# Kernel optimization log

Hardware: AMD Instinct MI355X
Metric: run time of the kernel (lower is better)

Reference implementation:

```python
import jax, jax.numpy as jnp
import numpy as np
import math

N_EMBD = 1024
N_HEAD = 16
BLOCK = 2048
SPARSITY = 0.25
B, T = 2, 2048


def _make_mask_logits(rng):
    # Replicates the patterned init in SparseMixtureAttention.__init__.
    S = BLOCK
    logits = np.empty((N_HEAD, S, S), dtype=np.float32)
    for h in range(N_HEAD):
        if h % 3 == 0:  # banded pattern (bandwidth 16)
            i = np.arange(S)
            band = (np.abs(i[:, None] - i[None, :]) <= 16)
            logits[h] = np.where(band, rng.standard_normal((S, S)) + 2.0,
                                 rng.standard_normal((S, S)) - 2.0)
        elif h % 3 == 1:  # strided pattern: every 4th column
            strided = (np.arange(S)[None, :] % 4 == 0)
            logits[h] = np.where(strided, rng.standard_normal((S, S)) + 2.0,
                                 rng.standard_normal((S, S)) - 2.0)
        else:  # random pattern with given sparsity
            rnd = rng.random((S, S)) < SPARSITY
            logits[h] = np.where(rnd, rng.standard_normal((S, S)) + 2.0,
                                 rng.standard_normal((S, S)) - 2.0)
    # keep the diagonal unmasked so no causal row is fully masked (avoids NaN rows)
    d = np.arange(S)
    logits[:, d, d] = np.abs(logits[:, d, d]) + 2.0
    return logits.astype(np.float32)


def setup_inputs() -> dict:
    key = jax.random.key(0)
    ks = jax.random.split(key, 5)
    rng = np.random.default_rng(0)
    return {
        "x": jax.random.normal(ks[0], (B, T, N_EMBD), dtype=jnp.float32),
        "mask_logits": jnp.asarray(_make_mask_logits(rng)),
        "W_attn": jax.random.normal(ks[1], (3 * N_EMBD, N_EMBD), dtype=jnp.float32) * 0.02,
        "b_attn": jnp.zeros((3 * N_EMBD,), dtype=jnp.float32),
        "W_proj": jax.random.normal(ks[2], (N_EMBD, N_EMBD), dtype=jnp.float32) * 0.02,
        "b_proj": jnp.zeros((N_EMBD,), dtype=jnp.float32),
    }


def reference(x, mask_logits, W_attn, b_attn, W_proj, b_proj):
    Bx, Tx, C = x.shape
    H = mask_logits.shape[0]
    D = C // H
    qkv = x @ W_attn.T + b_attn                       # [B,T,3C]
    q, k, v = jnp.split(qkv, 3, axis=-1)
    q = q.reshape(Bx, Tx, H, D)
    k = k.reshape(Bx, Tx, H, D)
    v = v.reshape(Bx, Tx, H, D)
    att = jnp.einsum('bthd,bshd->bhts', q, k) * (1.0 / math.sqrt(D))  # [B,H,T,T]
    # forward value of the STE mask equals the hard mask (probs - probs.detach() == 0)
    keep = jax.nn.sigmoid(mask_logits[:, :Tx, :Tx]) > 0.5             # [H,T,T]
    causal = jnp.tril(jnp.ones((Tx, Tx), dtype=bool))
    mask = causal[None, :, :] & keep                                  # [H,T,T]
    att = jnp.where(mask[None], att, -jnp.inf)
    att = jax.nn.softmax(att, axis=-1)
    y = jnp.einsum('bhts,bshd->bthd', att, v).reshape(Bx, Tx, C)
    return y @ W_proj.T + b_proj
```

## Files before the change

### kernel.cpp

```cpp
#include <hip/hip_runtime.h>
#include <hip/hip_bf16.h>
#include <stdint.h>

typedef unsigned short u16;
typedef unsigned int u32;
typedef unsigned long long u64;
typedef __attribute__((ext_vector_type(8))) short bf16x8;
typedef __attribute__((ext_vector_type(4))) float f32x4;

#define NB 2
#define NH 16
#define TT 2048
#define DD 64
#define CC 1024

__device__ __forceinline__ u16 bf16bits(float f) {
    __hip_bfloat16 h = __float2bfloat16(f);
    return __builtin_bit_cast(unsigned short, h);
}

__device__ __forceinline__ void gload_lds16(const void* g, void* l) {
    __builtin_amdgcn_global_load_lds(
        (const __attribute__((address_space(1))) void*)g,
        (__attribute__((address_space(3))) void*)l, 16, 0, 0);
}

__global__ __launch_bounds__(256) void prep_all(
    const float* __restrict__ x, const float* __restrict__ Wa_f,
    const float* __restrict__ Wp_f, const float* __restrict__ ml,
    u16* __restrict__ xb, u16* __restrict__ wab, u16* __restrict__ wpb,
    unsigned char* __restrict__ mb) {
    const int bid = blockIdx.x;
    if (bid < 512) {
        int idx = bid * 256 + threadIdx.x;
        for (int i = idx; i < 2097152; i += 512 * 256) {
            const float* src; u16* dst; int off;
            if (i < 1048576)      { src = x;    dst = xb;  off = i; }
            else if (i < 1835008) { src = Wa_f; dst = wab; off = i - 1048576; }
            else                  { src = Wp_f; dst = wpb; off = i - 1835008; }
            float4 v = reinterpret_cast<const float4*>(src)[off];
            ushort4 o;
            o.x = bf16bits(v.x); o.y = bf16bits(v.y);
            o.z = bf16bits(v.z); o.w = bf16bits(v.w);
            reinterpret_cast<ushort4*>(dst)[off] = o;
        }
    } else {
        const int wid = ((bid - 512) << 2) + (threadIdx.x >> 6);
        const int lane = threadIdx.x & 63;
        const int i0 = wid & 2047;
        const int hbase = (wid >> 11) << 3;
#pragma unroll 1
        for (int k = 0; k < 8; ++k) {
            int h = hbase + k;
            int i = (k & 1) ? (2047 - i0) : i0;
            int row = h * 2048 + i;
            const float* src = ml + (size_t)row * TT;
            unsigned char* dst = mb + (size_t)row * (TT / 8);
#pragma unroll 1
            for (int c8 = lane; c8 < 256; c8 += 64) {
                unsigned char v = 0;
                if (c8 * 8 <= i) {
                    const float4* p = reinterpret_cast<const float4*>(src + c8 * 8);
                    float4 a = p[0];
                    float4 b = p[1];
                    unsigned u = 0;
                    u |= (a.x > 0.f) ? 1u : 0u;
                    u |= (a.y > 0.f) ? 2u : 0u;
                    u |= (a.z > 0.f) ? 4u : 0u;
                    u |= (a.w > 0.f) ? 8u : 0u;
                    u |= (b.x > 0.f) ? 16u : 0u;
                    u |= (b.y > 0.f) ? 32u : 0u;
                    u |= (b.z > 0.f) ? 64u : 0u;
                    u |= (b.w > 0.f) ? 128u : 0u;
                    int rem = i - c8 * 8;
                    if (rem < 7) u &= (1u << (rem + 1)) - 1;
                    v = (unsigned char)u;
                }
                dst[c8] = v;
            }
        }
    }
}

template <int MODE>
__global__ __launch_bounds__(256) void gemm_bt(
    const u16* __restrict__ A, const u16* __restrict__ Bw,
    const float* __restrict__ bias,
    u16* __restrict__ Qb, u16* __restrict__ Kb, u16* __restrict__ Vtb,
    float* __restrict__ Cout, int Kdim) {
    const int bm = blockIdx.y * 128;
    const int bn = blockIdx.x * 128;
    const int tid = threadIdx.x;
    const int w = tid >> 6, lane = tid & 63;
    const int lrow = lane & 15, lgrp = lane >> 4;
    const int wr = (w >> 1) * 64, wc = (w & 1) * 64;

    __shared__ __align__(16) u16 ABs[2][128 * 64];
    u16* As = ABs[0];
    u16* Bs = ABs[1];

    f32x4 acc[4][4] = {};

    const int nkt = Kdim >> 6;
    for (int kt = 0; kt < nkt; ++kt) {
        const int k0 = kt << 6;
#pragma unroll
        for (int i = 0; i < 4; ++i) {
            int e = i * 2048 + tid * 8;
            int r = e >> 6, c = e & 63;
            gload_lds16(A + (size_t)(bm + r) * Kdim + k0 + c, (char*)As + i * 4096 + w * 1024);
            gload_lds16(Bw + (size_t)(bn + r) * Kdim + k0 + c, (char*)Bs + i * 4096 + w * 1024);
        }
        __syncthreads();
#pragma unroll
        for (int kk = 0; kk < 2; ++kk) {
            bf16x8 af[4], bfz[4];
#pragma unroll
            for (int i = 0; i < 4; ++i)
                af[i] = *reinterpret_cast<const bf16x8*>(&As[(wr + i * 16 + lrow) * 64 + kk * 32 + lgrp * 8]);
#pragma unroll
            for (int i = 0; i < 4; ++i)
                bfz[i] = *reinterpret_cast<const bf16x8*>(&Bs[(wc + i * 16 + lrow) * 64 + kk * 32 + lgrp * 8]);
#pragma unroll
            for (int mi = 0; mi < 4; ++mi)
#pragma unroll
                for (int ni = 0; ni < 4; ++ni)
                    acc[mi][ni] = __builtin_amdgcn_mfma_f32_16x16x32_bf16(af[mi], bfz[ni], acc[mi][ni], 0, 0, 0);
        }
        __syncthreads();
    }

    const int sec = (MODE == 0) ? (bn >> 10) : 1;

    if (MODE == 0 && sec == 2) {
        u16* Tl = &ABs[0][0];
#pragma unroll
        for (int ni = 0; ni < 4; ++ni) {
            int nl = wc + ni * 16 + lrow;
            float bv = bias[bn + nl];
#pragma unroll
            for (int mi = 0; mi < 4; ++mi) {
                int ml2 = wr + mi * 16 + lgrp * 4;
                u64 pk = 0;
#pragma unroll
                for (int j = 0; j < 4; ++j)
                    pk |= (u64)bf16bits(acc[mi][ni][j] + bv) << (16 * j);
                int byte = nl * 256 + ((ml2 * 2) ^ ((nl & 7) << 4));
                *reinterpret_cast<u64*>((char*)Tl + byte) = pk;
            }
        }
        __syncthreads();
        int r = tid >> 1, half = tid & 1;
        int h = ((bn & 1023) >> 6) + (r >> 6);
        int d = r & 63;
        int b = bm >> 11;
        u16* gdst = Vtb + (((size_t)b * NH + h) * DD + d) * TT + (bm & 2047) + half * 64;
#pragma unroll
        for (int c = 0; c < 8; ++c) {
            uint4 v = *reinterpret_cast<const uint4*>(
                (char*)Tl + r * 256 + ((half * 128 + c * 16) ^ ((r & 7) << 4)));
            *reinterpret_cast<uint4*>(gdst + c * 8) = v;
        }
        return;
    }

#pragma unroll
    for (int ni = 0; ni < 4; ++ni) {
        int n = bn + wc + ni * 16 + lrow;
        float bv = bias[n];
#pragma unroll
        for (int mi = 0; mi < 4; ++mi) {
#pragma unroll
            for (int j = 0; j < 4; ++j) {
                int m = bm + wr + mi * 16 + lgrp * 4 + j;
                float v = acc[mi][ni][j] + bv;
                if (MODE == 1) {
                    Cout[(size_t)m * 1024 + n] = v;
                } else {
                    int h = (n & 1023) >> 6;
                    int d = n & 63;
                    int b = m >> 11;
                    int t = m & 2047;
                    if (sec == 0) {
                        Qb[(((size_t)b * NH + h) * TT + t) * DD + d] =
                            bf16bits(v * (0.125f * 1.4426950408889634f));
                    } else {
                        Kb[(((size_t)b * NH + h) * TT + t) * DD + d] = bf16bits(v);
                    }
                }
            }
        }
    }
}

__global__ __launch_bounds__(256) void attn_kernel(
    const u16* __restrict__ Qb, const u16* __restrict__ Kb,
    const u16* __restrict__ Vtb, const unsigned char* __restrict__ mb,
    u16* __restrict__ att_out) {
    const int slot = blockIdx.x >> 4;
    const int h = blockIdx.x & 15;
    const int b = blockIdx.y;
    const int qt = (slot < 16) ? (31 - slot) : (slot - 16);
    const int tid = threadIdx.x;
    const int w = tid >> 6, lane = tid & 63;
    const int lrow = lane & 15, g = lane >> 4;

    __shared__ __align__(16) u16 Ks[2][64 * 64];
    __shared__ __align__(16) u16 Vts[2][64 * 64];
    __shared__ __align__(16) u16 Ps[4][16 * 64];

    const u16* kg_base = &Kb[((size_t)b * NH + h) * TT * DD];
    const u16* vg_base = &Vtb[((size_t)b * NH + h) * DD * TT];

    auto STAGE = [&](int bufi, int kt) {
#pragma unroll
        for (int i = 0; i < 2; ++i) {
            int e = i * 2048 + tid * 8;
            int r = e >> 6, c = e & 63;
            int cs = c ^ ((r & 7) << 3);
            gload_lds16(kg_base + (size_t)kt * 64 * DD + r * DD + cs,
                        (char*)Ks[bufi] + i * 4096 + w * 1024);
            gload_lds16(vg_base + kt * 64 + (size_t)r * TT + cs,
                        (char*)Vts[bufi] + i * 4096 + w * 1024);
        }
    };

    const int qrow_g = qt * 64 + w * 16 + lrow;
    const int rswz = (lrow & 7) << 4;

    bf16x8 qf[2];
#pragma unroll
    for (int kk = 0; kk < 2; ++kk)
        qf[kk] = *reinterpret_cast<const bf16x8*>(
            &Qb[(((size_t)b * NH + h) * TT + qrow_g) * DD + kk * 32 + g * 8]);

    f32x4 oacc[4] = {};
    float l_run = 0.f;

    const unsigned char* mrow_base = mb + ((size_t)h * TT + qrow_g) * (TT / 8);
    char* PsW = (char*)&Ps[w][0];

    STAGE(0, 0);
    int buf = 0;

#pragma unroll 1
    for (int kt = 0; kt <= qt; ++kt) {
        u64 mw = *reinterpret_cast<const u64*>(mrow_base + kt * 8);
        if (kt < qt) {
            STAGE(buf ^ 1, kt + 1);
            asm volatile("s_waitcnt vmcnt(5)" ::: "memory");
        } else {
            asm volatile("s_waitcnt vmcnt(1)" ::: "memory");
        }
        __builtin_amdgcn_sched_barrier(0);
        asm volatile("s_barrier" ::: "memory");

        f32x4 s[4] = {};
        __builtin_amdgcn_s_setprio(1);
#pragma unroll
        for (int kk = 0; kk < 2; ++kk)
#pragma unroll
            for (int nt = 0; nt < 4; ++nt) {
                bf16x8 kf = *reinterpret_cast<const bf16x8*>(
                    (char*)Ks[buf] + (((nt * 16 + lrow) * 128 + (kk * 32 + g * 8) * 2) ^ rswz));
                s[nt] = __builtin_amdgcn_mfma_f32_16x16x32_bf16(kf, qf[kk], s[nt], 0, 0, 0);
            }
        __builtin_amdgcn_s_setprio(0);

        u64 mws = mw >> (g * 4);
        u32 wlo = (u32)mws, whi = (u32)(mws >> 32);
        float rs = 0.f;
#pragma unroll
        for (int nt = 0; nt < 4; ++nt)
#pragma unroll
            for (int j = 0; j < 4; ++j) {
                int bi = nt * 16 + j;
                u32 word = (bi < 32) ? wlo : whi;
                u32 pm = (u32)(((int)(word << (31 - (bi & 31)))) >> 31);
                float p = __builtin_bit_cast(float,
                          __builtin_bit_cast(u32, exp2f(s[nt][j])) & pm);
                rs += p;
                s[nt][j] = p;
            }
        rs += __shfl_xor(rs, 16);
        rs += __shfl_xor(rs, 32);
        l_run += rs;

#pragma unroll
        for (int nt = 0; nt < 4; ++nt)
#pragma unroll
            for (int t = 0; t < 2; ++t) {
                u32 pk = (u32)bf16bits(s[nt][2 * t]) |
                         ((u32)bf16bits(s[nt][2 * t + 1]) << 16);
                int byte = (lrow * 128 + (nt * 16 + g * 4 + 2 * t) * 2) ^ rswz;
                *reinterpret_cast<u32*>(PsW + byte) = pk;
            }

        __builtin_amdgcn_s_setprio(1);
#pragma unroll
        for (int kk = 0; kk < 2; ++kk) {
            bf16x8 pf = *reinterpret_cast<const bf16x8*>(
                PsW + ((lrow * 128 + (kk * 32 + g * 8) * 2) ^ rswz));
#pragma unroll
            for (int dt = 0; dt < 4; ++dt) {
                bf16x8 vf = *reinterpret_cast<const bf16x8*>(
                    (char*)Vts[buf] + (((dt * 16 + lrow) * 128 + (kk * 32 + g * 8) * 2) ^ rswz));
                oacc[dt] = __builtin_amdgcn_mfma_f32_16x16x32_bf16(pf, vf, oacc[dt], 0, 0, 0);
            }
        }
        __builtin_amdgcn_s_setprio(0);

        asm volatile("s_barrier" ::: "memory");
        buf ^= 1;
    }

    float lb[4];
#pragma unroll
    for (int j = 0; j < 4; ++j)
        lb[j] = __shfl(l_run, (lane & 48) + g * 4 + j);
#pragma unroll
    for (int dt = 0; dt < 4; ++dt)
#pragma unroll
        for (int j = 0; j < 4; ++j) {
            int t = qt * 64 + w * 16 + g * 4 + j;
            float o = oacc[dt][j] / lb[j];
            att_out[((size_t)b * TT + t) * CC + h * DD + dt * 16 + lrow] = bf16bits(o);
        }
}

extern "C" void kernel_launch(void* const* d_in, const int* in_sizes, int n_in,
                              void* d_out, int out_size, void* d_ws, size_t ws_size,
                              hipStream_t stream) {
    const float* x = (const float*)d_in[0];
    const float* mask_logits = (const float*)d_in[1];
    const float* W_attn = (const float*)d_in[2];
    const float* b_attn = (const float*)d_in[3];
    const float* W_proj = (const float*)d_in[4];
    const float* b_proj = (const float*)d_in[5];
    float* out = (float*)d_out;

    char* ws = (char*)d_ws;
    u16* xb  = (u16*)(ws + 0);
    u16* Wa  = (u16*)(ws + (8u << 20));
    u16* Wp  = (u16*)(ws + (14u << 20));
    u16* Qb  = (u16*)(ws + (16u << 20));
    u16* Kb  = (u16*)(ws + (24u << 20));
    u16* Vtb = (u16*)(ws + (32u << 20));
    u16* att = (u16*)(ws + (40u << 20));
    unsigned char* mbits = (unsigned char*)(ws + (48u << 20));

    prep_all<<<1536, 256, 0, stream>>>(x, W_attn, W_proj, mask_logits,
                                       xb, Wa, Wp, mbits);
    gemm_bt<0><<<dim3(24, 32), 256, 0, stream>>>(xb, Wa, b_attn, Qb, Kb, Vtb, nullptr, CC);
    attn_kernel<<<dim3(512, 2), 256, 0, stream>>>(Qb, Kb, Vtb, mbits, att);
    gemm_bt<1><<<dim3(8, 32), 256, 0, stream>>>(att, Wp, b_proj, nullptr, nullptr, nullptr, out, CC);
}
```

Baseline: 161.4 us.

## Process two query tiles per block and split long causal rows across blocks

Each attention block now handles 128 query rows as two 64-row tiles that share each staged K/V tile, which halves K/V LDS staging per query row. Long causal rows (query chunks 8-15) are split across two blocks over the key range; these write unnormalised bf16 partial outputs and row sums to workspace, and a new combine kernel sums them and normalises. The aim is better load balance across 768 blocks and reuse of K/V loads. The cost is an extra kernel launch, extra bf16 rounding of the partials, and higher register pressure under the 3-waves launch bound. The partials reuse workspace regions that earlier kernels have already finished with.

```diff
diff --git a/kernel.cpp b/kernel.cpp
--- a/kernel.cpp
+++ b/kernel.cpp
@@ -17,6 +17,11 @@
 __device__ __forceinline__ u16 bf16bits(float f) {
     __hip_bfloat16 h = __float2bfloat16(f);
     return __builtin_bit_cast(unsigned short, h);
+}
+
+__device__ __forceinline__ float bf2f(u16 u) {
+    u32 x = (u32)u << 16;
+    return __builtin_bit_cast(float, x);
 }
 
 __device__ __forceinline__ void gload_lds16(const void* g, void* l) {
@@ -193,21 +198,28 @@
     }
 }
 
-__global__ __launch_bounds__(256) void attn_kernel(
+__global__ __launch_bounds__(256, 3) void attn_kernel(
     const u16* __restrict__ Qb, const u16* __restrict__ Kb,
     const u16* __restrict__ Vtb, const unsigned char* __restrict__ mb,
-    u16* __restrict__ att_out) {
-    const int slot = blockIdx.x >> 4;
-    const int h = blockIdx.x & 15;
-    const int b = blockIdx.y;
-    const int qt = (slot < 16) ? (31 - slot) : (slot - 16);
+    u16* __restrict__ att_out, u16* __restrict__ Opart,
+    float* __restrict__ lpart) {
+    const int bid = blockIdx.x;
+    const int slot = bid >> 5;
+    const int hb = bid & 31;
+    const int h = hb >> 1, b = hb & 1;
+    int qc, k0, k1, half = 0;
+    bool split;
+    if (slot < 8)       { qc = slot;             k0 = 0;      k1 = 2 * qc + 2; split = false; }
+    else if (slot < 16) { qc = 15 - (slot - 8);  k0 = 0;      k1 = qc + 1;     split = true; half = 0; }
+    else                { qc = 15 - (slot - 16); k0 = qc + 1; k1 = 2 * qc + 2; split = true; half = 1; }
+
     const int tid = threadIdx.x;
     const int w = tid >> 6, lane = tid & 63;
     const int lrow = lane & 15, g = lane >> 4;
 
     __shared__ __align__(16) u16 Ks[2][64 * 64];
     __shared__ __align__(16) u16 Vts[2][64 * 64];
-    __shared__ __align__(16) u16 Ps[4][16 * 64];
+    __shared__ __align__(16) u16 Ps[4][2][16 * 64];
 
     const u16* kg_base = &Kb[((size_t)b * NH + h) * TT * DD];
     const u16* vg_base = &Vtb[((size_t)b * NH + h) * DD * TT];
@@ -225,37 +237,45 @@
         }
     };
 
-    const int qrow_g = qt * 64 + w * 16 + lrow;
+    const int qrow0 = qc * 128 + w * 16 + lrow;
     const int rswz = (lrow & 7) << 4;
 
-    bf16x8 qf[2];
-#pragma unroll
-    for (int kk = 0; kk < 2; ++kk)
-        qf[kk] = *reinterpret_cast<const bf16x8*>(
-            &Qb[(((size_t)b * NH + h) * TT + qrow_g) * DD + kk * 32 + g * 8]);
-
-    f32x4 oacc[4] = {};
-    float l_run = 0.f;
-
-    const unsigned char* mrow_base = mb + ((size_t)h * TT + qrow_g) * (TT / 8);
-    char* PsW = (char*)&Ps[w][0];
-
-    STAGE(0, 0);
+    bf16x8 qf0[2], qf1[2];
+#pragma unroll
+    for (int kk = 0; kk < 2; ++kk) {
+        qf0[kk] = *reinterpret_cast<const bf16x8*>(
+            &Qb[(((size_t)b * NH + h) * TT + qrow0) * DD + kk * 32 + g * 8]);
+        qf1[kk] = *reinterpret_cast<const bf16x8*>(
+            &Qb[(((size_t)b * NH + h) * TT + qrow0 + 64) * DD + kk * 32 + g * 8]);
+    }
+
+    f32x4 oacc0[4] = {}, oacc1[4] = {};
+    float l0 = 0.f, l1 = 0.f;
+
+    const unsigned char* mrow0 = mb + ((size_t)h * TT + qrow0) * (TT / 8);
+    const unsigned char* mrow1 = mrow0 + (size_t)64 * (TT / 8);
+    char* PsW0 = (char*)&Ps[w][0][0];
+    char* PsW1 = (char*)&Ps[w][1][0];
+
+    STAGE(0, k0);
     int buf = 0;
 
 #pragma unroll 1
-    for (int kt = 0; kt <= qt; ++kt) {
-        u64 mw = *reinterpret_cast<const u64*>(mrow_base + kt * 8);
-        if (kt < qt) {
+    for (int kt = k0; kt < k1; ++kt) {
+        u64 mw0 = *reinterpret_cast<const u64*>(mrow0 + kt * 8);
+        u64 mw1 = *reinterpret_cast<const u64*>(mrow1 + kt * 8);
+        if (kt + 1 < k1) {
             STAGE(buf ^ 1, kt + 1);
-            asm volatile("s_waitcnt vmcnt(5)" ::: "memory");
+            asm volatile("s_waitcnt vmcnt(6)" ::: "memory");
         } else {
-            asm volatile("s_waitcnt vmcnt(1)" ::: "memory");
+            asm volatile("s_waitcnt vmcnt(2)" ::: "memory");
         }
         __builtin_amdgcn_sched_barrier(0);
         asm volatile("s_barrier" ::: "memory");
 
-        f32x4 s[4] = {};
+        const bool do0 = (kt <= 2 * qc);
+
+        f32x4 s0[4] = {}, s1[4] = {};
         __builtin_amdgcn_s_setprio(1);
 #pragma unroll
         for (int kk = 0; kk < 2; ++kk)
@@ -263,49 +283,84 @@
             for (int nt = 0; nt < 4; ++nt) {
                 bf16x8 kf = *reinterpret_cast<const bf16x8*>(
                     (char*)Ks[buf] + (((nt * 16 + lrow) * 128 + (kk * 32 + g * 8) * 2) ^ rswz));
-                s[nt] = __builtin_amdgcn_mfma_f32_16x16x32_bf16(kf, qf[kk], s[nt], 0, 0, 0);
+                if (do0) s0[nt] = __builtin_amdgcn_mfma_f32_16x16x32_bf16(kf, qf0[kk], s0[nt], 0, 0, 0);
+                s1[nt] = __builtin_amdgcn_mfma_f32_16x16x32_bf16(kf, qf1[kk], s1[nt], 0, 0, 0);
             }
         __builtin_amdgcn_s_setprio(0);
 
-        u64 mws = mw >> (g * 4);
-        u32 wlo = (u32)mws, whi = (u32)(mws >> 32);
-        float rs = 0.f;
-#pragma unroll
-        for (int nt = 0; nt < 4; ++nt)
-#pragma unroll
-            for (int j = 0; j < 4; ++j) {
-                int bi = nt * 16 + j;
-                u32 word = (bi < 32) ? wlo : whi;
-                u32 pm = (u32)(((int)(word << (31 - (bi & 31)))) >> 31);
-                float p = __builtin_bit_cast(float,
-                          __builtin_bit_cast(u32, exp2f(s[nt][j])) & pm);
-                rs += p;
-                s[nt][j] = p;
-            }
-        rs += __shfl_xor(rs, 16);
-        rs += __shfl_xor(rs, 32);
-        l_run += rs;
-
-#pragma unroll
-        for (int nt = 0; nt < 4; ++nt)
-#pragma unroll
-            for (int t = 0; t < 2; ++t) {
-                u32 pk = (u32)bf16bits(s[nt][2 * t]) |
-                         ((u32)bf16bits(s[nt][2 * t + 1]) << 16);
-                int byte = (lrow * 128 + (nt * 16 + g * 4 + 2 * t) * 2) ^ rswz;
-                *reinterpret_cast<u32*>(PsW + byte) = pk;
-            }
+        if (do0) {
+            u64 mws = mw0 >> (g * 4);
+            u32 wlo = (u32)mws, whi = (u32)(mws >> 32);
+            float rs = 0.f;
+#pragma unroll
+            for (int nt = 0; nt < 4; ++nt)
+#pragma unroll
+                for (int j = 0; j < 4; ++j) {
+                    int bi = nt * 16 + j;
+                    u32 word = (bi < 32) ? wlo : whi;
+                    u32 pm = (u32)(((int)(word << (31 - (bi & 31)))) >> 31);
+                    float p = __builtin_bit_cast(float,
+                              __builtin_bit_cast(u32, exp2f(s0[nt][j])) & pm);
+                    rs += p;
+                    s0[nt][j] = p;
+                }
+            rs += __shfl_xor(rs, 16);
+            rs += __shfl_xor(rs, 32);
+            l0 += rs;
+#pragma unroll
+            for (int nt = 0; nt < 4; ++nt)
+#pragma unroll
+                for (int t = 0; t < 2; ++t) {
+                    u32 pk = (u32)bf16bits(s0[nt][2 * t]) |
+                             ((u32)bf16bits(s0[nt][2 * t + 1]) << 16);
+                    int byte = (lrow * 128 + (nt * 16 + g * 4 + 2 * t) * 2) ^ rswz;
+                    *reinterpret_cast<u32*>(PsW0 + byte) = pk;
+                }
+        }
+
+        {
+            u64 mws = mw1 >> (g * 4);
+            u32 wlo = (u32)mws, whi = (u32)(mws >> 32);
+            float rs = 0.f;
+#pragma unroll
+            for (int nt = 0; nt < 4; ++nt)
+#pragma unroll
+                for (int j = 0; j < 4; ++j) {
+                    int bi = nt * 16 + j;
+                    u32 word = (bi < 32) ? wlo : whi;
+                    u32 pm = (u32)(((int)(word << (31 - (bi & 31)))) >> 31);
+                    float p = __builtin_bit_cast(float,
+                              __builtin_bit_cast(u32, exp2f(s1[nt][j])) & pm);
+                    rs += p;
+                    s1[nt][j] = p;
+                }
+            rs += __shfl_xor(rs, 16);
+            rs += __shfl_xor(rs, 32);
+            l1 += rs;
+#pragma unroll
+            for (int nt = 0; nt < 4; ++nt)
+#pragma unroll
+                for (int t = 0; t < 2; ++t) {
+                    u32 pk = (u32)bf16bits(s1[nt][2 * t]) |
+                             ((u32)bf16bits(s1[nt][2 * t + 1]) << 16);
+                    int byte = (lrow * 128 + (nt * 16 + g * 4 + 2 * t) * 2) ^ rswz;
+                    *reinterpret_cast<u32*>(PsW1 + byte) = pk;
+                }
+        }
 
         __builtin_amdgcn_s_setprio(1);
 #pragma unroll
         for (int kk = 0; kk < 2; ++kk) {
-            bf16x8 pf = *reinterpret_cast<const bf16x8*>(
-                PsW + ((lrow * 128 + (kk * 32 + g * 8) * 2) ^ rswz));
+            int pb = (lrow * 128 + (kk * 32 + g * 8) * 2) ^ rswz;
+            bf16x8 pf0;
+            if (do0) pf0 = *reinterpret_cast<const bf16x8*>(PsW0 + pb);
+            bf16x8 pf1 = *reinterpret_cast<const bf16x8*>(PsW1 + pb);
 #pragma unroll
             for (int dt = 0; dt < 4; ++dt) {
                 bf16x8 vf = *reinterpret_cast<const bf16x8*>(
                     (char*)Vts[buf] + (((dt * 16 + lrow) * 128 + (kk * 32 + g * 8) * 2) ^ rswz));
-                oacc[dt] = __builtin_amdgcn_mfma_f32_16x16x32_bf16(pf, vf, oacc[dt], 0, 0, 0);
+                if (do0) oacc0[dt] = __builtin_amdgcn_mfma_f32_16x16x32_bf16(pf0, vf, oacc0[dt], 0, 0, 0);
+                oacc1[dt] = __builtin_amdgcn_mfma_f32_16x16x32_bf16(pf1, vf, oacc1[dt], 0, 0, 0);
             }
         }
         __builtin_amdgcn_s_setprio(0);
@@ -314,18 +369,66 @@
         buf ^= 1;
     }
 
-    float lb[4];
-#pragma unroll
-    for (int j = 0; j < 4; ++j)
-        lb[j] = __shfl(l_run, (lane & 48) + g * 4 + j);
-#pragma unroll
-    for (int dt = 0; dt < 4; ++dt)
+    if (!split) {
+        float lb0[4], lb1[4];
 #pragma unroll
         for (int j = 0; j < 4; ++j) {
-            int t = qt * 64 + w * 16 + g * 4 + j;
-            float o = oacc[dt][j] / lb[j];
-            att_out[((size_t)b * TT + t) * CC + h * DD + dt * 16 + lrow] = bf16bits(o);
-        }
+            lb0[j] = __shfl(l0, (lane & 48) + g * 4 + j);
+            lb1[j] = __shfl(l1, (lane & 48) + g * 4 + j);
+        }
+#pragma unroll
+        for (int dt = 0; dt < 4; ++dt)
+#pragma unroll
+            for (int j = 0; j < 4; ++j) {
+                int t = qc * 128 + w * 16 + g * 4 + j;
+                att_out[((size_t)b * TT + t) * CC + h * DD + dt * 16 + lrow] =
+                    bf16bits(oacc0[dt][j] / lb0[j]);
+                att_out[((size_t)b * TT + t + 64) * CC + h * DD + dt * 16 + lrow] =
+                    bf16bits(oacc1[dt][j] / lb1[j]);
+            }
+    } else {
+        const int cid = (hb << 3) + (qc - 8);
+        u16* Op = Opart + (size_t)(cid * 2 + half) * 8192;
+#pragma unroll
+        for (int dt = 0; dt < 4; ++dt)
+#pragma unroll
+            for (int j = 0; j < 4; ++j) {
+                int r0 = w * 16 + g * 4 + j;
+                Op[r0 * 64 + dt * 16 + lrow] = bf16bits(oacc0[dt][j]);
+                Op[(r0 + 64) * 64 + dt * 16 + lrow] = bf16bits(oacc1[dt][j]);
+            }
+        if (g == 0) {
+            lpart[(size_t)(cid * 2 + half) * 128 + w * 16 + lrow] = l0;
+            lpart[(size_t)(cid * 2 + half) * 128 + 64 + w * 16 + lrow] = l1;
+        }
+    }
+}
+
+__global__ __launch_bounds__(256) void combine_kernel(
+    const u16* __restrict__ Opart, const float* __restrict__ lpart,
+    u16* __restrict__ att_out) {
+    const int cid = blockIdx.x;
+    const int hb = cid >> 3;
+    const int h = hb >> 1, b = hb & 1;
+    const int qc = 8 + (cid & 7);
+    const int t = threadIdx.x;
+    const int row = t >> 1, c0 = (t & 1) << 5;
+
+    const u16* p0 = Opart + (size_t)(cid * 2) * 8192 + row * 64 + c0;
+    const u16* p1 = p0 + 8192;
+    float l = lpart[(size_t)(cid * 2) * 128 + row] +
+              lpart[(size_t)(cid * 2 + 1) * 128 + row];
+    float inv = 1.0f / l;
+
+    u16 ov[32];
+#pragma unroll
+    for (int i = 0; i < 32; ++i)
+        ov[i] = bf16bits((bf2f(p0[i]) + bf2f(p1[i])) * inv);
+
+    u16* dst = att_out + ((size_t)b * TT + qc * 128 + row) * CC + h * DD + c0;
+#pragma unroll
+    for (int i = 0; i < 4; ++i)
+        reinterpret_cast<uint4*>(dst)[i] = reinterpret_cast<const uint4*>(ov)[i];
 }
 
 extern "C" void kernel_launch(void* const* d_in, const int* in_sizes, int n_in,
@@ -348,10 +451,13 @@
     u16* Vtb = (u16*)(ws + (32u << 20));
     u16* att = (u16*)(ws + (40u << 20));
     unsigned char* mbits = (unsigned char*)(ws + (48u << 20));
+    u16* Opart = (u16*)(ws + 0);
+    float* lpart = (float*)(ws + (8u << 20));
 
     prep_all<<<1536, 256, 0, stream>>>(x, W_attn, W_proj, mask_logits,
                                        xb, Wa, Wp, mbits);
     gemm_bt<0><<<dim3(24, 32), 256, 0, stream>>>(xb, Wa, b_attn, Qb, Kb, Vtb, nullptr, CC);
-    attn_kernel<<<dim3(512, 2), 256, 0, stream>>>(Qb, Kb, Vtb, mbits, att);
+    attn_kernel<<<768, 256, 0, stream>>>(Qb, Kb, Vtb, mbits, att, Opart, lpart);
+    combine_kernel<<<256, 256, 0, stream>>>(Opart, lpart, att);
     gemm_bt<1><<<dim3(8, 32), 256, 0, stream>>>(att, Wp, b_proj, nullptr, nullptr, nullptr, out, CC);
 }
```

Result: slower. 170.0 us (+5.3%).
